# Optimization experiments

Measured on AMD Instinct MI355X. Metric: run time of the kernel, lower is better.

The kernel has to match this reference:

```python
import jax, jax.numpy as jnp
import numpy as np

IOU_THRESHOLD = 0.5
NEGATIVE_RATIO = 3
ALPHA = 1.0
B, A, D, G = 64, 8732, 85, 32  # batch, anchors, 4+81 classes, max gt per image


def cxcywh_to_xyxy(b):
    cx, cy, w, h = b[..., 0], b[..., 1], b[..., 2], b[..., 3]
    return jnp.stack([cx - w / 2, cy - h / 2, cx + w / 2, cy + h / 2], axis=-1)


def box_iou(a, b):
    # a: (G,4) xyxy, b: (A,4) xyxy -> (G,A)
    lt = jnp.maximum(a[:, None, :2], b[None, :, :2])
    rb = jnp.minimum(a[:, None, 2:], b[None, :, 2:])
    wh = jnp.clip(rb - lt, 0.0)
    inter = wh[..., 0] * wh[..., 1]
    area_a = (a[:, 2] - a[:, 0]) * (a[:, 3] - a[:, 1])
    area_b = (b[:, 2] - b[:, 0]) * (b[:, 3] - b[:, 1])
    return inter / (area_a[:, None] + area_b[None, :] - inter)


def encode(gt, anchors):
    g_cxcy = (gt[:, :2] - anchors[:, :2]) / anchors[:, 2:]
    g_wh = jnp.log(gt[:, 2:]) - jnp.log(anchors[:, 2:])
    return jnp.concatenate([g_cxcy, g_wh], axis=-1)


def match_one(gt_box, gt_label, count, anchors):
    # gt_box (G,4) cxcywh, gt_label (G,), count scalar, anchors (A,4) cxcywh
    num_anchors = anchors.shape[0]
    valid = jnp.arange(gt_box.shape[0]) < count
    iou = box_iou(cxcywh_to_xyxy(gt_box), cxcywh_to_xyxy(anchors))  # (G,A)
    iou = jnp.where(valid[:, None], iou, -1.0)
    best_gt_overlap = iou.max(0)
    best_gt_idx = iou.argmax(0)
    over = best_gt_overlap > IOU_THRESHOLD
    loc = jnp.where(over[:, None], encode(gt_box[best_gt_idx], anchors), 0.0)
    cls = jnp.where(over, gt_label[best_gt_idx].astype(jnp.float32) + 1.0, 0.0)
    # force-match: each (valid) gt claims its best anchor, overwriting
    best_prior_idx = iou.argmax(1)  # (G,)
    idx = jnp.where(valid, best_prior_idx, num_anchors)  # dump invalid gt into a scratch row
    loc = jnp.concatenate([loc, jnp.zeros((1, 4), loc.dtype)], 0)
    loc = loc.at[idx].set(encode(gt_box, anchors[best_prior_idx]))[:num_anchors]
    cls = jnp.concatenate([cls, jnp.zeros((1,), cls.dtype)], 0)
    cls = cls.at[idx].set(gt_label.astype(jnp.float32) + 1.0)[:num_anchors]
    return loc, cls


def smooth_l1(d):
    ad = jnp.abs(d)
    return jnp.where(ad < 1.0, 0.5 * d * d, ad - 0.5)


def multibox_loss(pred, anchors, gt_boxes, gt_labels, gt_counts):
    num_anchors = pred.shape[1]
    loc_pred, conf_pred = pred[:, :, :4], pred[:, :, 4:]
    target_loc, target_cls = jax.vmap(match_one, in_axes=(0, 0, 0, None))(
        gt_boxes, gt_labels, gt_counts, anchors)  # (B,A,4), (B,A)
    pos = target_cls > 0  # (B,A)
    posf = pos.astype(pred.dtype)
    n_pos = posf.sum(1)  # (B,) guaranteed > 0 since every image has >=1 gt
    # localization: per-element smooth-L1 on positives, normalized per image
    loc_l = smooth_l1(loc_pred - target_loc) * posf[:, :, None]
    loc_loss = jnp.sum(loc_l / n_pos[:, None, None])
    # classification CE per anchor
    logp = jax.nn.log_softmax(conf_pred, axis=-1)  # (B,A,C)
    cls_ce = -jnp.take_along_axis(logp, target_cls.astype(jnp.int32)[:, :, None], axis=-1)[..., 0]
    pos_loss = jnp.sum(cls_ce * posf / n_pos[:, None])
    # hard negative mining (double-sort rank trick, no grad through selection)
    num_neg = jnp.minimum(NEGATIVE_RATIO * pos.sum(1), num_anchors - 1)  # (B,) int
    all_neg = jax.lax.stop_gradient(jnp.where(pos, 0.0, cls_ce))
    order = jnp.argsort(-all_neg, axis=1)
    rank = jnp.argsort(order, axis=1)
    neg_mask = (rank < num_neg[:, None]).astype(pred.dtype)
    neg_ce = -logp[:, :, 0]  # CE against background class 0
    neg_loss = jnp.sum(neg_ce * neg_mask / n_pos[:, None])
    return ALPHA * loc_loss + pos_loss + neg_loss


def setup_inputs() -> dict:
    key = jax.random.key(0)
    k1, k2, k3, k4, k5, k6, k7 = jax.random.split(key, 7)
    pred = jax.random.normal(k1, (B, A, D), dtype=jnp.float32)
    anchors = jnp.concatenate([
        jax.random.uniform(k2, (A, 2), minval=0.0, maxval=1.0),
        jax.random.uniform(k3, (A, 2), minval=0.05, maxval=0.5)], axis=-1)
    gt_boxes = jnp.concatenate([
        jax.random.uniform(k4, (B, G, 2), minval=0.0, maxval=1.0),
        jax.random.uniform(k5, (B, G, 2), minval=0.05, maxval=0.6)], axis=-1)
    gt_labels = jax.random.randint(k6, (B, G), 0, 80)
    gt_counts = jax.random.randint(k7, (B,), 1, G + 1)
    return {"pred": pred, "anchors": anchors, "gt_boxes": gt_boxes,
            "gt_labels": gt_labels, "gt_counts": gt_counts}


def reference(pred, anchors, gt_boxes, gt_labels, gt_counts):
    return multibox_loss(pred, anchors, gt_boxes, gt_labels, gt_counts)
```

## Files before the change

kernel.cpp:

```cpp
#include <hip/hip_runtime.h>
#include <math.h>

#define BB 64
#define AA 8732
#define DD 85
#define GG 32
#define CC 81
#define TILE 64
#define NT 137
#define TPB 12
#define NTB 12
#define NAB 35
#define BLKANCH (TPB * TILE)


typedef __attribute__((address_space(3))) unsigned int lds_u32;
typedef const __attribute__((address_space(1))) unsigned int glb_u32;

__device__ __forceinline__ float smoothl1(float d) {
  float ad = fabsf(d);
  return ad < 1.0f ? 0.5f * d * d : ad - 0.5f;
}

__device__ __forceinline__ float frcp(float x) {
  return __builtin_amdgcn_rcpf(x);
}

__global__ __launch_bounds__(256) void k_match(
    const float* __restrict__ anchors, const float* __restrict__ gt_boxes,
    const int* __restrict__ gt_counts, int* __restrict__ match,
    int* __restrict__ bestp, int* __restrict__ n_pos, int* __restrict__ done_sel)
{
  const int b = blockIdx.y;
  const int count = gt_counts[b];
  __shared__ float gx0[GG], gy0[GG], gx1[GG], gy1[GG], gar[GG];
  __shared__ float wv[4];
  __shared__ int wi[4];

  if (blockIdx.x < NAB) {
    if (blockIdx.x == 0 && threadIdx.x == 0) {
      n_pos[b] = 0;
      if (b == 0) *done_sel = 0;
    }
    if (threadIdx.x < GG) {
      float4 gb = reinterpret_cast<const float4*>(gt_boxes)[b * GG + threadIdx.x];
      float x0 = gb.x - gb.z * 0.5f, y0 = gb.y - gb.w * 0.5f;
      float x1 = gb.x + gb.z * 0.5f, y1 = gb.y + gb.w * 0.5f;
      gx0[threadIdx.x] = x0; gy0[threadIdx.x] = y0;
      gx1[threadIdx.x] = x1; gy1[threadIdx.x] = y1;
      gar[threadIdx.x] = (x1 - x0) * (y1 - y0);
    }
    __syncthreads();
    const int a = blockIdx.x * 256 + threadIdx.x;
    if (a < AA) {
      float4 an = reinterpret_cast<const float4*>(anchors)[a];
      float ax0 = an.x - an.z * 0.5f, ay0 = an.y - an.w * 0.5f;
      float ax1 = an.x + an.z * 0.5f, ay1 = an.y + an.w * 0.5f;
      float aar = (ax1 - ax0) * (ay1 - ay0);
      float best = -1.0f; int bi = 0;
      for (int g = 0; g < count; ++g) {
        float iw = fmaxf(fminf(gx1[g], ax1) - fmaxf(gx0[g], ax0), 0.0f);
        float ih = fmaxf(fminf(gy1[g], ay1) - fmaxf(gy0[g], ay0), 0.0f);
        float inter = iw * ih;
        float iou = inter * frcp(gar[g] + aar - inter);
        if (iou > best) { best = iou; bi = g; }
      }
      match[b * AA + a] = (best > 0.5f) ? bi : -1;
    }
  } else {
    const int g = blockIdx.x - NAB;
    if (g < count) {
      float4 gb = reinterpret_cast<const float4*>(gt_boxes)[b * GG + g];
      const float gx0s = gb.x - gb.z * 0.5f, gy0s = gb.y - gb.w * 0.5f;
      const float gx1s = gb.x + gb.z * 0.5f, gy1s = gb.y + gb.w * 0.5f;
      const float gars = (gx1s - gx0s) * (gy1s - gy0s);

      float bv = -2.0f; int bi = AA;
      for (int a = threadIdx.x; a < AA; a += 256) {
        float4 an = reinterpret_cast<const float4*>(anchors)[a];
        float ax0 = an.x - an.z * 0.5f, ay0 = an.y - an.w * 0.5f;
        float ax1 = an.x + an.z * 0.5f, ay1 = an.y + an.w * 0.5f;
        float aar = (ax1 - ax0) * (ay1 - ay0);
        float iw = fmaxf(fminf(gx1s, ax1) - fmaxf(gx0s, ax0), 0.0f);
        float ih = fmaxf(fminf(gy1s, ay1) - fmaxf(gy0s, ay0), 0.0f);
        float inter = iw * ih;
        float iou = inter * frcp(gars + aar - inter);
        if (iou > bv || (iou == bv && a < bi)) { bv = iou; bi = a; }
      }
      #pragma unroll
      for (int m = 1; m < 64; m <<= 1) {
        float ov = __shfl_xor(bv, m);
        int   oi = __shfl_xor(bi, m);
        if (ov > bv || (ov == bv && oi < bi)) { bv = ov; bi = oi; }
      }
      if ((threadIdx.x & 63) == 0) { wv[threadIdx.x >> 6] = bv; wi[threadIdx.x >> 6] = bi; }
      __syncthreads();
      if (threadIdx.x == 0) {
        float fv = wv[0]; int fi = wi[0];
        #pragma unroll
        for (int w = 1; w < 4; ++w)
          if (wv[w] > fv || (wv[w] == fv && wi[w] < fi)) { fv = wv[w]; fi = wi[w]; }
        bestp[b * GG + g] = fi;
      }
    }
  }
}

__global__ __launch_bounds__(256) void k_loss(
    const float* __restrict__ pred, const float* __restrict__ anchors,
    const float* __restrict__ gt_boxes, const int* __restrict__ gt_labels,
    const int* __restrict__ gt_counts, const int* __restrict__ match,
    const int* __restrict__ bestp, float* __restrict__ all_neg,
    float* __restrict__ partials, int* __restrict__ n_pos)
{
  const int b = blockIdx.y;
  const int t0 = blockIdx.x * TPB;
  const int t1 = min(t0 + TPB, NT);
  const int abase = t0 * TILE;
  const int tid = threadIdx.x;
  __shared__ float bufs[2][TILE * DD];
  __shared__ int ovrblk[BLKANCH];
  __shared__ int slab[GG];
  __shared__ float wsum[4];
  __shared__ int wcnt[4];

  if (tid < GG) slab[tid] = gt_labels[b * GG + tid];
  for (int i = tid; i < BLKANCH; i += 256) ovrblk[i] = -1;

  #define PREFETCH(t, bufp)                                                  \
    do {                                                                     \
      const int a0_ = (t) * TILE;                                            \
      const int nch_ = (min(TILE, AA - a0_) * DD) >> 2;                      \
      const float* s_ = pred + ((size_t)b * AA + a0_) * DD;                  \
      _Pragma("unroll")                                                      \
      for (int j_ = 0; j_ < 6; ++j_) {                                       \
        int c_ = j_ * 256 + tid;                                             \
        if (c_ < nch_)                                                       \
          __builtin_amdgcn_global_load_lds(                                  \
              (glb_u32*)(s_ + c_ * 4), (lds_u32*)((bufp) + c_ * 4), 16, 0, 0);\
      }                                                                      \
    } while (0)

  PREFETCH(t0, &bufs[0][0]);
  __syncthreads();

  if (tid < GG && tid < gt_counts[b]) {
    int p = bestp[b * GG + tid];
    if (p >= abase && p < abase + BLKANCH) atomicMax(&ovrblk[p - abase], tid);
  }
  __syncthreads();

  const int r = tid >> 2;
  const int sub = tid & 3;
  float acc = 0.0f;
  int poscnt = 0;
  int cur = 0;

  for (int t = t0; t < t1; ++t) {
    if (t + 1 < t1) {
      PREFETCH(t + 1, &bufs[cur ^ 1][0]);
      __builtin_amdgcn_sched_barrier(0);
    }

    const int a0 = t * TILE;
    const int nr = min(TILE, AA - a0);
    const float* rows = &bufs[cur][0];

    if (r < nr) {
      const int a = a0 + r;
      int m = match[b * AA + a];
      { int o = ovrblk[a - abase]; if (o >= 0) m = o; }

      const float* row = rows + r * DD + 4;
      float v[21];
      float mx = -INFINITY;
      #pragma unroll
      for (int k = 0; k < 21; ++k) {
        const int cc = 4 * k + sub;
        float x = (cc < CC) ? row[cc] : -INFINITY;
        v[k] = x;
        mx = fmaxf(mx, x);
      }
      #pragma unroll
      for (int msk = 1; msk <= 2; msk <<= 1)
        mx = fmaxf(mx, __shfl_xor(mx, msk));
      float s = 0.0f;
      #pragma unroll
      for (int k = 0; k < 21; ++k) s += __expf(v[k] - mx);
      #pragma unroll
      for (int msk = 1; msk <= 2; msk <<= 1) s += __shfl_xor(s, msk);
      const float lse = mx + __logf(s);

      if (sub == 0) {
        if (m >= 0) {
          poscnt += 1;
          const int tgt = slab[m] + 1;
          float cls_ce = lse - row[tgt];
          float4 an = reinterpret_cast<const float4*>(anchors)[a];
          float4 gb = reinterpret_cast<const float4*>(gt_boxes)[b * GG + m];
          float tx = (gb.x - an.x) / an.z;
          float ty = (gb.y - an.y) / an.w;
          float tw = __logf(gb.z) - __logf(an.z);
          float th = __logf(gb.w) - __logf(an.w);
          acc += smoothl1(rows[r * DD + 0] - tx)
               + smoothl1(rows[r * DD + 1] - ty)
               + smoothl1(rows[r * DD + 2] - tw)
               + smoothl1(rows[r * DD + 3] - th)
               + cls_ce;
          all_neg[b * AA + a] = 0.0f;
        } else {
          float ce = lse - row[0];
          all_neg[b * AA + a] = fmaxf(ce, 0.0f);
        }
      }
    }

    __syncthreads();
    cur ^= 1;
  }

  #pragma unroll
  for (int msk = 1; msk < 64; msk <<= 1) {
    acc    += __shfl_xor(acc, msk);
    poscnt += __shfl_xor(poscnt, msk);
  }
  if ((tid & 63) == 0) {
    wsum[tid >> 6] = acc;
    wcnt[tid >> 6] = poscnt;
  }
  __syncthreads();
  if (tid == 0) {
    partials[b * NTB + blockIdx.x] = (wsum[0] + wsum[1]) + (wsum[2] + wsum[3]);
    int c = wcnt[0] + wcnt[1] + wcnt[2] + wcnt[3];
    if (c) atomicAdd(&n_pos[b], c);
  }
  #undef PREFETCH
}

__global__ __launch_bounds__(1024) void k_select(
    const float* __restrict__ all_neg, const float* __restrict__ partials,
    const int* __restrict__ n_pos, float* __restrict__ batch_total,
    int* __restrict__ done_sel, float* __restrict__ out)
{
  const int b = blockIdx.x;
  const int tid = threadIdx.x;
  __shared__ unsigned u[AA];
  __shared__ int hist16[16][257];
  __shared__ int hist[256];
  __shared__ unsigned sh_pref;
  __shared__ int sh_k;
  __shared__ int sflag;
  __shared__ float wf[16];
  __shared__ int wc[16];

  {
    const float* srcg = all_neg + (size_t)b * AA;
    #pragma unroll
    for (int j = 0; j < 3; ++j) {
      int c = j * 1024 + tid;
      if (c < 2183)
        __builtin_amdgcn_global_load_lds(
            (glb_u32*)(srcg + c * 4), (lds_u32*)((float*)u + c * 4), 16, 0, 0);
    }
  }

  float ps = 0.0f;
  if (tid < 16) {
    float pv = (tid < NTB) ? partials[b * NTB + tid] : 0.0f;
    #pragma unroll
    for (int m = 1; m < 16; m <<= 1) pv += __shfl_xor(pv, m);
    ps = pv;
  }
  __syncthreads();

  const int np = n_pos[b];
  const int K = min(3 * np, AA - 1);
  const int wvid = tid >> 6;

  unsigned prefix = 0;
  int kk = K;
  for (int shift = 24; shift >= 0; shift -= 8) {
    int* hflat = &hist16[0][0];
    for (int i = tid; i < 16 * 257; i += 1024) hflat[i] = 0;
    __syncthreads();
    const unsigned hmask = (shift == 24) ? 0u : (0xFFFFFFFFu << (shift + 8));
    for (int i = tid; i < AA; i += 1024) {
      unsigned x = u[i];
      if ((x & hmask) == prefix)
        atomicAdd(&hist16[wvid][(x >> shift) & 255], 1);
    }
    __syncthreads();
    if (tid < 256) {
      int s = 0;
      #pragma unroll
      for (int h = 0; h < 16; ++h) s += hist16[h][tid];
      hist[tid] = s;
    }
    __syncthreads();
    #pragma unroll
    for (int off = 1; off < 256; off <<= 1) {
      int v = 0;
      if (tid < 256) v = hist[tid] + ((tid + off < 256) ? hist[tid + off] : 0);
      __syncthreads();
      if (tid < 256) hist[tid] = v;
      __syncthreads();
    }
    if (tid < 256) {
      int s_here = hist[tid];
      int s_next = (tid < 255) ? hist[tid + 1] : 0;
      if (s_here >= kk && s_next < kk) {
        sh_pref = prefix | ((unsigned)tid << shift);
        sh_k = kk - s_next;
      }
    }
    __syncthreads();
    prefix = sh_pref;
    kk = sh_k;
    __syncthreads();
  }
  const float tstar = __uint_as_float(prefix);

  float ssum = 0.0f; int cgt = 0;
  for (int i = tid; i < AA; i += 1024) {
    float x = __uint_as_float(u[i]);
    if (x > tstar) { ssum += x; cgt += 1; }
  }
  #pragma unroll
  for (int m = 1; m < 64; m <<= 1) {
    ssum += __shfl_xor(ssum, m);
    cgt  += __shfl_xor(cgt, m);
  }
  if ((tid & 63) == 0) { wf[wvid] = ssum; wc[wvid] = cgt; }
  __syncthreads();
  if (tid == 0) {
    float S = 0.0f; int Cg = 0;
    #pragma unroll
    for (int w = 0; w < 16; ++w) { S += wf[w]; Cg += wc[w]; }
    float neg_sum = S + (float)(K - Cg) * tstar;
    batch_total[b] = (ps + neg_sum) / (float)np;
    __threadfence();
    int old = atomicAdd(done_sel, 1);
    sflag = (old == BB - 1) ? 1 : 0;
  }
  __syncthreads();

  if (sflag) {
    __threadfence();
    if (tid < 64) {
      float v = batch_total[tid];
      #pragma unroll
      for (int m = 1; m < 64; m <<= 1) v += __shfl_xor(v, m);
      if (tid == 0) out[0] = v;
    }
  }
}

extern "C" void kernel_launch(void* const* d_in, const int* in_sizes, int n_in,
                              void* d_out, int out_size, void* d_ws, size_t ws_size,
                              hipStream_t stream) {
  (void)in_sizes; (void)n_in; (void)out_size; (void)ws_size;
  const float* pred      = (const float*)d_in[0];
  const float* anchors   = (const float*)d_in[1];
  const float* gt_boxes  = (const float*)d_in[2];
  const int*   gt_labels = (const int*)d_in[3];
  const int*   gt_counts = (const int*)d_in[4];

  char* ws = (char*)d_ws;
  int*   match       = (int*)(ws + 0);
  float* all_neg     = (float*)(ws + 2235392);
  float* partials    = (float*)(ws + 4470784);
  float* batch_total = (float*)(ws + 4473856);
  int*   bestp       = (int*)(ws + 4474112);
  int*   n_pos       = (int*)(ws + 4482304);
  int*   done_sel    = (int*)(ws + 4482560);
  float* out = (float*)d_out;

  hipLaunchKernelGGL(k_match, dim3(NAB + GG, BB), dim3(256), 0, stream,
                     anchors, gt_boxes, gt_counts, match, bestp, n_pos, done_sel);
  hipLaunchKernelGGL(k_loss, dim3(NTB, BB), dim3(256), 0, stream,
                     pred, anchors, gt_boxes, gt_labels, gt_counts, match, bestp,
                     all_neg, partials, n_pos);
  hipLaunchKernelGGL(k_select, dim3(BB), dim3(1024), 0, stream,
                     all_neg, partials, n_pos, batch_total, done_sel, out);
}
```

Measured before the change: 88.04 us.

## Fuse per-anchor IoU matching into loss kernel and deepen tile prefetch pipeline

Moves the per-anchor best-gt IoU computation out of the match kernel and into the loss kernel. There it is split across 4 lanes with a shuffle argmax, so the match array no longer makes a round trip through global memory. Anchors and gt boxes are staged in LDS, and the loss grid changes to 8 blocks of 18 tiles each. Full blocks use two-tile-ahead prefetch with explicit vmcnt waits. The select kernel's 256-bin suffix scan is replaced by a single-wave shuffle scan, cutting barriers. The trade-off is extra IoU work inside the bandwidth-bound loss loop, fewer blocks in total, and more LDS per block, which may lower occupancy.

```diff
diff --git a/kernel.cpp b/kernel.cpp
--- a/kernel.cpp
+++ b/kernel.cpp
@@ -8,9 +8,8 @@
 #define CC 81
 #define TILE 64
 #define NT 137
-#define TPB 12
-#define NTB 12
-#define NAB 35
+#define TPB 18
+#define NTB 8
 #define BLKANCH (TPB * TILE)
 
 
@@ -28,106 +27,98 @@
 
 __global__ __launch_bounds__(256) void k_match(
     const float* __restrict__ anchors, const float* __restrict__ gt_boxes,
-    const int* __restrict__ gt_counts, int* __restrict__ match,
-    int* __restrict__ bestp, int* __restrict__ n_pos, int* __restrict__ done_sel)
+    const int* __restrict__ gt_counts, int* __restrict__ bestp,
+    int* __restrict__ n_pos, int* __restrict__ done_sel)
 {
+  const int g = blockIdx.x;
   const int b = blockIdx.y;
+  if (g == 0 && threadIdx.x == 0) {
+    n_pos[b] = 0;
+    if (b == 0) *done_sel = 0;
+  }
   const int count = gt_counts[b];
-  __shared__ float gx0[GG], gy0[GG], gx1[GG], gy1[GG], gar[GG];
+  if (g >= count) return;
+
   __shared__ float wv[4];
   __shared__ int wi[4];
 
-  if (blockIdx.x < NAB) {
-    if (blockIdx.x == 0 && threadIdx.x == 0) {
-      n_pos[b] = 0;
-      if (b == 0) *done_sel = 0;
-    }
-    if (threadIdx.x < GG) {
-      float4 gb = reinterpret_cast<const float4*>(gt_boxes)[b * GG + threadIdx.x];
-      float x0 = gb.x - gb.z * 0.5f, y0 = gb.y - gb.w * 0.5f;
-      float x1 = gb.x + gb.z * 0.5f, y1 = gb.y + gb.w * 0.5f;
-      gx0[threadIdx.x] = x0; gy0[threadIdx.x] = y0;
-      gx1[threadIdx.x] = x1; gy1[threadIdx.x] = y1;
-      gar[threadIdx.x] = (x1 - x0) * (y1 - y0);
-    }
-    __syncthreads();
-    const int a = blockIdx.x * 256 + threadIdx.x;
-    if (a < AA) {
-      float4 an = reinterpret_cast<const float4*>(anchors)[a];
-      float ax0 = an.x - an.z * 0.5f, ay0 = an.y - an.w * 0.5f;
-      float ax1 = an.x + an.z * 0.5f, ay1 = an.y + an.w * 0.5f;
-      float aar = (ax1 - ax0) * (ay1 - ay0);
-      float best = -1.0f; int bi = 0;
-      for (int g = 0; g < count; ++g) {
-        float iw = fmaxf(fminf(gx1[g], ax1) - fmaxf(gx0[g], ax0), 0.0f);
-        float ih = fmaxf(fminf(gy1[g], ay1) - fmaxf(gy0[g], ay0), 0.0f);
-        float inter = iw * ih;
-        float iou = inter * frcp(gar[g] + aar - inter);
-        if (iou > best) { best = iou; bi = g; }
-      }
-      match[b * AA + a] = (best > 0.5f) ? bi : -1;
-    }
-  } else {
-    const int g = blockIdx.x - NAB;
-    if (g < count) {
-      float4 gb = reinterpret_cast<const float4*>(gt_boxes)[b * GG + g];
-      const float gx0s = gb.x - gb.z * 0.5f, gy0s = gb.y - gb.w * 0.5f;
-      const float gx1s = gb.x + gb.z * 0.5f, gy1s = gb.y + gb.w * 0.5f;
-      const float gars = (gx1s - gx0s) * (gy1s - gy0s);
-
-      float bv = -2.0f; int bi = AA;
-      for (int a = threadIdx.x; a < AA; a += 256) {
-        float4 an = reinterpret_cast<const float4*>(anchors)[a];
-        float ax0 = an.x - an.z * 0.5f, ay0 = an.y - an.w * 0.5f;
-        float ax1 = an.x + an.z * 0.5f, ay1 = an.y + an.w * 0.5f;
-        float aar = (ax1 - ax0) * (ay1 - ay0);
-        float iw = fmaxf(fminf(gx1s, ax1) - fmaxf(gx0s, ax0), 0.0f);
-        float ih = fmaxf(fminf(gy1s, ay1) - fmaxf(gy0s, ay0), 0.0f);
-        float inter = iw * ih;
-        float iou = inter * frcp(gars + aar - inter);
-        if (iou > bv || (iou == bv && a < bi)) { bv = iou; bi = a; }
-      }
-      #pragma unroll
-      for (int m = 1; m < 64; m <<= 1) {
-        float ov = __shfl_xor(bv, m);
-        int   oi = __shfl_xor(bi, m);
-        if (ov > bv || (ov == bv && oi < bi)) { bv = ov; bi = oi; }
-      }
-      if ((threadIdx.x & 63) == 0) { wv[threadIdx.x >> 6] = bv; wi[threadIdx.x >> 6] = bi; }
-      __syncthreads();
-      if (threadIdx.x == 0) {
-        float fv = wv[0]; int fi = wi[0];
-        #pragma unroll
-        for (int w = 1; w < 4; ++w)
-          if (wv[w] > fv || (wv[w] == fv && wi[w] < fi)) { fv = wv[w]; fi = wi[w]; }
-        bestp[b * GG + g] = fi;
-      }
-    }
+  float4 gb = reinterpret_cast<const float4*>(gt_boxes)[b * GG + g];
+  const float gx0s = gb.x - gb.z * 0.5f, gy0s = gb.y - gb.w * 0.5f;
+  const float gx1s = gb.x + gb.z * 0.5f, gy1s = gb.y + gb.w * 0.5f;
+  const float gars = (gx1s - gx0s) * (gy1s - gy0s);
+
+  float bv = -2.0f; int bi = AA;
+  for (int a = threadIdx.x; a < AA; a += 256) {
+    float4 an = reinterpret_cast<const float4*>(anchors)[a];
+    float ax0 = an.x - an.z * 0.5f, ay0 = an.y - an.w * 0.5f;
+    float ax1 = an.x + an.z * 0.5f, ay1 = an.y + an.w * 0.5f;
+    float aar = (ax1 - ax0) * (ay1 - ay0);
+    float iw = fmaxf(fminf(gx1s, ax1) - fmaxf(gx0s, ax0), 0.0f);
+    float ih = fmaxf(fminf(gy1s, ay1) - fmaxf(gy0s, ay0), 0.0f);
+    float inter = iw * ih;
+    float iou = inter * frcp(gars + aar - inter);
+    if (iou > bv || (iou == bv && a < bi)) { bv = iou; bi = a; }
+  }
+  #pragma unroll
+  for (int m = 1; m < 64; m <<= 1) {
+    float ov = __shfl_xor(bv, m);
+    int   oi = __shfl_xor(bi, m);
+    if (ov > bv || (ov == bv && oi < bi)) { bv = ov; bi = oi; }
+  }
+  if ((threadIdx.x & 63) == 0) { wv[threadIdx.x >> 6] = bv; wi[threadIdx.x >> 6] = bi; }
+  __syncthreads();
+  if (threadIdx.x == 0) {
+    float fv = wv[0]; int fi = wi[0];
+    #pragma unroll
+    for (int w = 1; w < 4; ++w)
+      if (wv[w] > fv || (wv[w] == fv && wi[w] < fi)) { fv = wv[w]; fi = wi[w]; }
+    bestp[b * GG + g] = fi;
   }
 }
 
 __global__ __launch_bounds__(256) void k_loss(
     const float* __restrict__ pred, const float* __restrict__ anchors,
     const float* __restrict__ gt_boxes, const int* __restrict__ gt_labels,
-    const int* __restrict__ gt_counts, const int* __restrict__ match,
-    const int* __restrict__ bestp, float* __restrict__ all_neg,
-    float* __restrict__ partials, int* __restrict__ n_pos)
+    const int* __restrict__ gt_counts, const int* __restrict__ bestp,
+    float* __restrict__ all_neg, float* __restrict__ partials,
+    int* __restrict__ n_pos)
 {
   const int b = blockIdx.y;
   const int t0 = blockIdx.x * TPB;
   const int t1 = min(t0 + TPB, NT);
   const int abase = t0 * TILE;
+  const int nanch = min(BLKANCH, AA - abase);
   const int tid = threadIdx.x;
+  const bool fast = (blockIdx.x < NTB - 1);
+
   __shared__ float bufs[2][TILE * DD];
-  __shared__ int ovrblk[BLKANCH];
+  __shared__ float4 anch[BLKANCH];
+  __shared__ int ovr[BLKANCH];
+  __shared__ float sgx0[GG], sgy0[GG], sgx1[GG], sgy1[GG], sgar[GG];
+  __shared__ float4 sgb[GG];
   __shared__ int slab[GG];
   __shared__ float wsum[4];
   __shared__ int wcnt[4];
 
-  if (tid < GG) slab[tid] = gt_labels[b * GG + tid];
-  for (int i = tid; i < BLKANCH; i += 256) ovrblk[i] = -1;
-
-  #define PREFETCH(t, bufp)                                                  \
+  const int cnt = gt_counts[b];
+
+  if (tid < GG) {
+    float4 gb = reinterpret_cast<const float4*>(gt_boxes)[b * GG + tid];
+    sgb[tid] = gb;
+    float x0 = gb.x - gb.z * 0.5f, y0 = gb.y - gb.w * 0.5f;
+    float x1 = gb.x + gb.z * 0.5f, y1 = gb.y + gb.w * 0.5f;
+    sgx0[tid] = x0; sgy0[tid] = y0; sgx1[tid] = x1; sgy1[tid] = y1;
+    sgar[tid] = (x1 - x0) * (y1 - y0);
+    slab[tid] = gt_labels[b * GG + tid];
+  }
+  for (int i = tid; i < BLKANCH; i += 256) ovr[i] = -1;
+  __syncthreads();
+  if (tid < GG && tid < cnt) {
+    int p = bestp[b * GG + tid];
+    if (p >= abase && p < abase + nanch) atomicMax(&ovr[p - abase], tid);
+  }
+
+  #define PF_TILE(t, bufp)                                                   \
     do {                                                                     \
       const int a0_ = (t) * TILE;                                            \
       const int nch_ = (min(TILE, AA - a0_) * DD) >> 2;                      \
@@ -141,14 +132,18 @@
       }                                                                      \
     } while (0)
 
-  PREFETCH(t0, &bufs[0][0]);
-  __syncthreads();
-
-  if (tid < GG && tid < gt_counts[b]) {
-    int p = bestp[b * GG + tid];
-    if (p >= abase && p < abase + BLKANCH) atomicMax(&ovrblk[p - abase], tid);
-  }
-  __syncthreads();
+  #define PF_ANCH()                                                          \
+    do {                                                                     \
+      const float* s_ = anchors + (size_t)abase * 4;                         \
+      float* d_ = (float*)&anch[0];                                          \
+      _Pragma("unroll")                                                      \
+      for (int j_ = 0; j_ < 5; ++j_) {                                       \
+        int c_ = j_ * 256 + tid;                                             \
+        if (c_ < nanch)                                                      \
+          __builtin_amdgcn_global_load_lds(                                  \
+              (glb_u32*)(s_ + c_ * 4), (lds_u32*)(d_ + c_ * 4), 16, 0, 0);   \
+      }                                                                      \
+    } while (0)
 
   const int r = tid >> 2;
   const int sub = tid & 3;
@@ -156,20 +151,34 @@
   int poscnt = 0;
   int cur = 0;
 
-  for (int t = t0; t < t1; ++t) {
-    if (t + 1 < t1) {
-      PREFETCH(t + 1, &bufs[cur ^ 1][0]);
-      __builtin_amdgcn_sched_barrier(0);
-    }
-
+  auto compute_tile = [&](int t, int cur_) {
     const int a0 = t * TILE;
     const int nr = min(TILE, AA - a0);
-    const float* rows = &bufs[cur][0];
-
+    const float* rows = &bufs[cur_][0];
     if (r < nr) {
       const int a = a0 + r;
-      int m = match[b * AA + a];
-      { int o = ovrblk[a - abase]; if (o >= 0) m = o; }
+      const int ai = a - abase;
+      float4 an = anch[ai];
+      float ax0 = an.x - an.z * 0.5f, ay0 = an.y - an.w * 0.5f;
+      float ax1 = an.x + an.z * 0.5f, ay1 = an.y + an.w * 0.5f;
+      float aar = (ax1 - ax0) * (ay1 - ay0);
+
+      float bv = -1.0f; int bg = 0;
+      for (int g = sub; g < cnt; g += 4) {
+        float iw = fmaxf(fminf(sgx1[g], ax1) - fmaxf(sgx0[g], ax0), 0.0f);
+        float ih = fmaxf(fminf(sgy1[g], ay1) - fmaxf(sgy0[g], ay0), 0.0f);
+        float inter = iw * ih;
+        float iou = inter * frcp(sgar[g] + aar - inter);
+        if (iou > bv) { bv = iou; bg = g; }
+      }
+      #pragma unroll
+      for (int msk = 1; msk <= 2; msk <<= 1) {
+        float ov = __shfl_xor(bv, msk);
+        int   og = __shfl_xor(bg, msk);
+        if (ov > bv || (ov == bv && og < bg)) { bv = ov; bg = og; }
+      }
+      int m = (bv > 0.5f) ? bg : -1;
+      { int o = ovr[ai]; if (o >= 0) m = o; }
 
       const float* row = rows + r * DD + 4;
       float v[21];
@@ -196,8 +205,7 @@
           poscnt += 1;
           const int tgt = slab[m] + 1;
           float cls_ce = lse - row[tgt];
-          float4 an = reinterpret_cast<const float4*>(anchors)[a];
-          float4 gb = reinterpret_cast<const float4*>(gt_boxes)[b * GG + m];
+          float4 gb = sgb[m];
           float tx = (gb.x - an.x) / an.z;
           float ty = (gb.y - an.y) / an.w;
           float tw = __logf(gb.z) - __logf(an.z);
@@ -214,9 +222,42 @@
         }
       }
     }
-
-    __syncthreads();
-    cur ^= 1;
+  };
+
+  if (fast) {
+    PF_ANCH();
+    PF_TILE(t0, &bufs[0][0]);
+    PF_TILE(t0 + 1, &bufs[1][0]);
+    asm volatile("s_waitcnt vmcnt(5) lgkmcnt(0)" ::: "memory");
+    __builtin_amdgcn_s_barrier();
+
+    for (int t = t0; t < t1; ++t) {
+      compute_tile(t, cur);
+      if (t + 1 < t1) {
+        __builtin_amdgcn_s_barrier();
+        if (t + 2 < t1) {
+          PF_TILE(t + 2, &bufs[cur][0]);
+          asm volatile("s_waitcnt vmcnt(5) lgkmcnt(0)" ::: "memory");
+        } else {
+          asm volatile("s_waitcnt vmcnt(0) lgkmcnt(0)" ::: "memory");
+        }
+        __builtin_amdgcn_s_barrier();
+        cur ^= 1;
+      }
+    }
+  } else {
+    PF_ANCH();
+    PF_TILE(t0, &bufs[0][0]);
+    __syncthreads();
+    for (int t = t0; t < t1; ++t) {
+      if (t + 1 < t1) {
+        PF_TILE(t + 1, &bufs[cur ^ 1][0]);
+        __builtin_amdgcn_sched_barrier(0);
+      }
+      compute_tile(t, cur);
+      __syncthreads();
+      cur ^= 1;
+    }
   }
 
   #pragma unroll
@@ -234,7 +275,8 @@
     int c = wcnt[0] + wcnt[1] + wcnt[2] + wcnt[3];
     if (c) atomicAdd(&n_pos[b], c);
   }
-  #undef PREFETCH
+  #undef PF_TILE
+  #undef PF_ANCH
 }
 
 __global__ __launch_bounds__(1024) void k_select(
@@ -265,10 +307,10 @@
   }
 
   float ps = 0.0f;
-  if (tid < 16) {
-    float pv = (tid < NTB) ? partials[b * NTB + tid] : 0.0f;
+  if (tid < NTB) {
+    float pv = partials[b * NTB + tid];
     #pragma unroll
-    for (int m = 1; m < 16; m <<= 1) pv += __shfl_xor(pv, m);
+    for (int m = 1; m < NTB; m <<= 1) pv += __shfl_xor(pv, m);
     ps = pv;
   }
   __syncthreads();
@@ -297,21 +339,22 @@
       hist[tid] = s;
     }
     __syncthreads();
-    #pragma unroll
-    for (int off = 1; off < 256; off <<= 1) {
-      int v = 0;
-      if (tid < 256) v = hist[tid] + ((tid + off < 256) ? hist[tid + off] : 0);
-      __syncthreads();
-      if (tid < 256) hist[tid] = v;
-      __syncthreads();
-    }
-    if (tid < 256) {
-      int s_here = hist[tid];
-      int s_next = (tid < 255) ? hist[tid + 1] : 0;
-      if (s_here >= kk && s_next < kk) {
-        sh_pref = prefix | ((unsigned)tid << shift);
-        sh_k = kk - s_next;
-      }
+    if (tid < 64) {
+      int h0 = hist[4 * tid], h1 = hist[4 * tid + 1];
+      int h2 = hist[4 * tid + 2], h3 = hist[4 * tid + 3];
+      int lsum = h0 + h1 + h2 + h3;
+      int suf = lsum;
+      #pragma unroll
+      for (int off = 1; off < 64; off <<= 1) {
+        int o = __shfl_down(suf, off);
+        suf += (tid + off < 64) ? o : 0;
+      }
+      int after = suf - lsum;
+      int s3 = h3 + after, s2 = h2 + s3, s1 = h1 + s2, s0 = h0 + s1;
+      if (s0 >= kk && s1 < kk)    { sh_pref = prefix | ((unsigned)(4*tid+0) << shift); sh_k = kk - s1; }
+      if (s1 >= kk && s2 < kk)    { sh_pref = prefix | ((unsigned)(4*tid+1) << shift); sh_k = kk - s2; }
+      if (s2 >= kk && s3 < kk)    { sh_pref = prefix | ((unsigned)(4*tid+2) << shift); sh_k = kk - s3; }
+      if (s3 >= kk && after < kk) { sh_pref = prefix | ((unsigned)(4*tid+3) << shift); sh_k = kk - after; }
     }
     __syncthreads();
     prefix = sh_pref;
@@ -366,19 +409,18 @@
   const int*   gt_counts = (const int*)d_in[4];
 
   char* ws = (char*)d_ws;
-  int*   match       = (int*)(ws + 0);
-  float* all_neg     = (float*)(ws + 2235392);
-  float* partials    = (float*)(ws + 4470784);
-  float* batch_total = (float*)(ws + 4473856);
-  int*   bestp       = (int*)(ws + 4474112);
-  int*   n_pos       = (int*)(ws + 4482304);
-  int*   done_sel    = (int*)(ws + 4482560);
+  float* all_neg     = (float*)(ws + 0);
+  float* partials    = (float*)(ws + 2235392);
+  float* batch_total = (float*)(ws + 2237440);
+  int*   bestp       = (int*)(ws + 2237696);
+  int*   n_pos       = (int*)(ws + 2245888);
+  int*   done_sel    = (int*)(ws + 2246144);
   float* out = (float*)d_out;
 
-  hipLaunchKernelGGL(k_match, dim3(NAB + GG, BB), dim3(256), 0, stream,
-                     anchors, gt_boxes, gt_counts, match, bestp, n_pos, done_sel);
+  hipLaunchKernelGGL(k_match, dim3(GG, BB), dim3(256), 0, stream,
+                     anchors, gt_boxes, gt_counts, bestp, n_pos, done_sel);
   hipLaunchKernelGGL(k_loss, dim3(NTB, BB), dim3(256), 0, stream,
-                     pred, anchors, gt_boxes, gt_labels, gt_counts, match, bestp,
+                     pred, anchors, gt_boxes, gt_labels, gt_counts, bestp,
                      all_neg, partials, n_pos);
   hipLaunchKernelGGL(k_select, dim3(BB), dim3(1024), 0, stream,
                      all_neg, partials, n_pos, batch_total, done_sel, out);
```

Result: slower. 100.8 us (+14.5%).

## Load pred rows directly into registers and use wave-level scan in select

Applied to the files above, without the earlier changes.

The loss kernel drops the double-buffered LDS staging of pred tiles and has each lane load float4 chunks of its anchor row straight from global memory into registers. The target logit is picked during the max scan, and gt boxes are cached in shared memory. The grid changes to 18 blocks of 8 tiles per image, so the partials reduction widens accordingly. In k_select, the 256-entry histogram suffix scan moves from a multi-barrier LDS scan to a single-wave shuffle scan. The unaligned 340-byte row stride may make the float4 loads less efficient than the async LDS copies.

```diff
diff --git a/kernel.cpp b/kernel.cpp
--- a/kernel.cpp
+++ b/kernel.cpp
@@ -7,11 +7,9 @@
 #define GG 32
 #define CC 81
 #define TILE 64
-#define NT 137
-#define TPB 12
-#define NTB 12
+#define RPB 8
+#define NTB 18
 #define NAB 35
-#define BLKANCH (TPB * TILE)
 
 
 typedef __attribute__((address_space(3))) unsigned int lds_u32;
@@ -114,39 +112,25 @@
     float* __restrict__ partials, int* __restrict__ n_pos)
 {
   const int b = blockIdx.y;
-  const int t0 = blockIdx.x * TPB;
-  const int t1 = min(t0 + TPB, NT);
-  const int abase = t0 * TILE;
+  const int abase = blockIdx.x * RPB * TILE;
   const int tid = threadIdx.x;
-  __shared__ float bufs[2][TILE * DD];
-  __shared__ int ovrblk[BLKANCH];
+  __shared__ int ovr[RPB * TILE];
+  __shared__ float4 sgb[GG];
   __shared__ int slab[GG];
   __shared__ float wsum[4];
   __shared__ int wcnt[4];
 
-  if (tid < GG) slab[tid] = gt_labels[b * GG + tid];
-  for (int i = tid; i < BLKANCH; i += 256) ovrblk[i] = -1;
-
-  #define PREFETCH(t, bufp)                                                  \
-    do {                                                                     \
-      const int a0_ = (t) * TILE;                                            \
-      const int nch_ = (min(TILE, AA - a0_) * DD) >> 2;                      \
-      const float* s_ = pred + ((size_t)b * AA + a0_) * DD;                  \
-      _Pragma("unroll")                                                      \
-      for (int j_ = 0; j_ < 6; ++j_) {                                       \
-        int c_ = j_ * 256 + tid;                                             \
-        if (c_ < nch_)                                                       \
-          __builtin_amdgcn_global_load_lds(                                  \
-              (glb_u32*)(s_ + c_ * 4), (lds_u32*)((bufp) + c_ * 4), 16, 0, 0);\
-      }                                                                      \
-    } while (0)
-
-  PREFETCH(t0, &bufs[0][0]);
-  __syncthreads();
-
-  if (tid < GG && tid < gt_counts[b]) {
+  const int cnt = gt_counts[b];
+  if (tid < GG) {
+    sgb[tid] = reinterpret_cast<const float4*>(gt_boxes)[b * GG + tid];
+    slab[tid] = gt_labels[b * GG + tid];
+  }
+  ovr[tid] = -1; ovr[tid + 256] = -1;
+  __syncthreads();
+  if (tid < GG && tid < cnt) {
     int p = bestp[b * GG + tid];
-    if (p >= abase && p < abase + BLKANCH) atomicMax(&ovrblk[p - abase], tid);
+    int rel = p - abase;
+    if (rel >= 0 && rel < RPB * TILE) atomicMax(&ovr[rel], tid);
   }
   __syncthreads();
 
@@ -154,69 +138,77 @@
   const int sub = tid & 3;
   float acc = 0.0f;
   int poscnt = 0;
-  int cur = 0;
-
-  for (int t = t0; t < t1; ++t) {
-    if (t + 1 < t1) {
-      PREFETCH(t + 1, &bufs[cur ^ 1][0]);
-      __builtin_amdgcn_sched_barrier(0);
-    }
-
-    const int a0 = t * TILE;
-    const int nr = min(TILE, AA - a0);
-    const float* rows = &bufs[cur][0];
-
-    if (r < nr) {
-      const int a = a0 + r;
+
+  for (int i = 0; i < RPB; ++i) {
+    const int a0 = abase + i * TILE;
+    if (a0 >= AA) break;
+    const int a = a0 + r;
+    if (a < AA) {
+      const float* base = pred + ((size_t)b * AA + a) * DD;
+      float4 s0 = *(const float4*)(base + (sub)      * 4);
+      float4 s1 = *(const float4*)(base + (sub + 4)  * 4);
+      float4 s2 = *(const float4*)(base + (sub + 8)  * 4);
+      float4 s3 = *(const float4*)(base + (sub + 12) * 4);
+      float4 s4 = *(const float4*)(base + (sub + 16) * 4);
+      float4 s5f = make_float4(0.f, 0.f, 0.f, 0.f);
+      float  s5x = 0.0f;
+      if (sub == 0) s5f = *(const float4*)(base + 80);
+      if (sub == 1) s5x = base[84];
+
       int m = match[b * AA + a];
-      { int o = ovrblk[a - abase]; if (o >= 0) m = o; }
-
-      const float* row = rows + r * DD + 4;
-      float v[21];
-      float mx = -INFINITY;
-      #pragma unroll
-      for (int k = 0; k < 21; ++k) {
-        const int cc = 4 * k + sub;
-        float x = (cc < CC) ? row[cc] : -INFINITY;
-        v[k] = x;
-        mx = fmaxf(mx, x);
-      }
+      { int o = ovr[a - abase]; if (o >= 0) m = o; }
+      const int tgt = (m >= 0) ? slab[m] + 1 : 0;
+
+      const int cb = 4 * sub - 4;
+      float mx = -INFINITY, xt = -INFINITY;
+      #define SCAN(v, ccb)                                                   \
+        { mx = fmaxf(fmaxf(fmaxf(mx, (v).x), (v).y), fmaxf((v).z, (v).w));   \
+          if ((ccb) + 0 == tgt) xt = (v).x;                                  \
+          if ((ccb) + 1 == tgt) xt = (v).y;                                  \
+          if ((ccb) + 2 == tgt) xt = (v).z;                                  \
+          if ((ccb) + 3 == tgt) xt = (v).w; }
+      if (sub > 0) SCAN(s0, cb);
+      SCAN(s1, cb + 16); SCAN(s2, cb + 32); SCAN(s3, cb + 48); SCAN(s4, cb + 64);
+      if (sub == 0) SCAN(s5f, 76);
+      if (sub == 1) { mx = fmaxf(mx, s5x); if (tgt == 80) xt = s5x; }
+      #undef SCAN
       #pragma unroll
       for (int msk = 1; msk <= 2; msk <<= 1)
         mx = fmaxf(mx, __shfl_xor(mx, msk));
+
       float s = 0.0f;
-      #pragma unroll
-      for (int k = 0; k < 21; ++k) s += __expf(v[k] - mx);
-      #pragma unroll
-      for (int msk = 1; msk <= 2; msk <<= 1) s += __shfl_xor(s, msk);
+      #define ESUM(v) s += __expf((v).x - mx) + __expf((v).y - mx) +          \
+                           __expf((v).z - mx) + __expf((v).w - mx);
+      if (sub > 0) ESUM(s0);
+      ESUM(s1); ESUM(s2); ESUM(s3); ESUM(s4);
+      if (sub == 0) ESUM(s5f);
+      if (sub == 1) s += __expf(s5x - mx);
+      #undef ESUM
+      #pragma unroll
+      for (int msk = 1; msk <= 2; msk <<= 1) {
+        s  += __shfl_xor(s, msk);
+        xt  = fmaxf(xt, __shfl_xor(xt, msk));
+      }
       const float lse = mx + __logf(s);
+      const float ce = lse - xt;
 
       if (sub == 0) {
         if (m >= 0) {
           poscnt += 1;
-          const int tgt = slab[m] + 1;
-          float cls_ce = lse - row[tgt];
           float4 an = reinterpret_cast<const float4*>(anchors)[a];
-          float4 gb = reinterpret_cast<const float4*>(gt_boxes)[b * GG + m];
+          float4 gb = sgb[m];
           float tx = (gb.x - an.x) / an.z;
           float ty = (gb.y - an.y) / an.w;
           float tw = __logf(gb.z) - __logf(an.z);
           float th = __logf(gb.w) - __logf(an.w);
-          acc += smoothl1(rows[r * DD + 0] - tx)
-               + smoothl1(rows[r * DD + 1] - ty)
-               + smoothl1(rows[r * DD + 2] - tw)
-               + smoothl1(rows[r * DD + 3] - th)
-               + cls_ce;
+          acc += smoothl1(s0.x - tx) + smoothl1(s0.y - ty)
+               + smoothl1(s0.z - tw) + smoothl1(s0.w - th) + ce;
           all_neg[b * AA + a] = 0.0f;
         } else {
-          float ce = lse - row[0];
           all_neg[b * AA + a] = fmaxf(ce, 0.0f);
         }
       }
     }
-
-    __syncthreads();
-    cur ^= 1;
   }
 
   #pragma unroll
@@ -234,7 +226,6 @@
     int c = wcnt[0] + wcnt[1] + wcnt[2] + wcnt[3];
     if (c) atomicAdd(&n_pos[b], c);
   }
-  #undef PREFETCH
 }
 
 __global__ __launch_bounds__(1024) void k_select(
@@ -265,10 +256,10 @@
   }
 
   float ps = 0.0f;
-  if (tid < 16) {
+  if (tid < 64) {
     float pv = (tid < NTB) ? partials[b * NTB + tid] : 0.0f;
     #pragma unroll
-    for (int m = 1; m < 16; m <<= 1) pv += __shfl_xor(pv, m);
+    for (int m = 1; m < 32; m <<= 1) pv += __shfl_xor(pv, m);
     ps = pv;
   }
   __syncthreads();
@@ -297,21 +288,22 @@
       hist[tid] = s;
     }
     __syncthreads();
-    #pragma unroll
-    for (int off = 1; off < 256; off <<= 1) {
-      int v = 0;
-      if (tid < 256) v = hist[tid] + ((tid + off < 256) ? hist[tid + off] : 0);
-      __syncthreads();
-      if (tid < 256) hist[tid] = v;
-      __syncthreads();
-    }
-    if (tid < 256) {
-      int s_here = hist[tid];
-      int s_next = (tid < 255) ? hist[tid + 1] : 0;
-      if (s_here >= kk && s_next < kk) {
-        sh_pref = prefix | ((unsigned)tid << shift);
-        sh_k = kk - s_next;
-      }
+    if (tid < 64) {
+      int h0 = hist[4 * tid], h1 = hist[4 * tid + 1];
+      int h2 = hist[4 * tid + 2], h3 = hist[4 * tid + 3];
+      int lsum = h0 + h1 + h2 + h3;
+      int suf = lsum;
+      #pragma unroll
+      for (int off = 1; off < 64; off <<= 1) {
+        int o = __shfl_down(suf, off);
+        suf += (tid + off < 64) ? o : 0;
+      }
+      int after = suf - lsum;
+      int s3 = h3 + after, s2 = h2 + s3, s1 = h1 + s2, s0 = h0 + s1;
+      if (s0 >= kk && s1 < kk)    { sh_pref = prefix | ((unsigned)(4*tid+0) << shift); sh_k = kk - s1; }
+      if (s1 >= kk && s2 < kk)    { sh_pref = prefix | ((unsigned)(4*tid+1) << shift); sh_k = kk - s2; }
+      if (s2 >= kk && s3 < kk)    { sh_pref = prefix | ((unsigned)(4*tid+2) << shift); sh_k = kk - s3; }
+      if (s3 >= kk && after < kk) { sh_pref = prefix | ((unsigned)(4*tid+3) << shift); sh_k = kk - after; }
     }
     __syncthreads();
     prefix = sh_pref;
@@ -369,10 +361,10 @@
   int*   match       = (int*)(ws + 0);
   float* all_neg     = (float*)(ws + 2235392);
   float* partials    = (float*)(ws + 4470784);
-  float* batch_total = (float*)(ws + 4473856);
-  int*   bestp       = (int*)(ws + 4474112);
-  int*   n_pos       = (int*)(ws + 4482304);
-  int*   done_sel    = (int*)(ws + 4482560);
+  float* batch_total = (float*)(ws + 4475392);
+  int*   bestp       = (int*)(ws + 4475648);
+  int*   n_pos       = (int*)(ws + 4483840);
+  int*   done_sel    = (int*)(ws + 4484096);
   float* out = (float*)d_out;
 
   hipLaunchKernelGGL(k_match, dim3(NAB + GG, BB), dim3(256), 0, stream,
```

Result: faster. 84.52 us (-4.0%).
